# Kernel optimization log

Measured on AMD Instinct MI355X. Metric: run time of the kernel, lower is better.

## Reference

```python
import jax, jax.numpy as jnp
import numpy as np

N, E, SEQ, IN, HID, OUT = 2048, 65536, 5, 32, 64, 16
EPS = 1e-5


def setup_inputs() -> dict:
    ks = jax.random.split(jax.random.key(0), 16)
    def w(k, shape):
        return jax.random.normal(k, shape, jnp.float32) / np.float32(np.sqrt(shape[0]))
    z = lambda n: jnp.zeros((n,), jnp.float32)
    return dict(
        x=jax.random.normal(ks[0], (SEQ, N, IN), jnp.float32),
        edge_weight=jax.random.uniform(ks[1], (E,), jnp.float32),
        Wcz=w(ks[2], (IN, HID)), bcz=z(HID), Wlz=w(ks[3], (2 * HID, HID)), blz=z(HID),
        Wcr=w(ks[4], (IN, HID)), bcr=z(HID), Wlr=w(ks[5], (2 * HID, HID)), blr=z(HID),
        Wch=w(ks[6], (IN, HID)), bch=z(HID), Wlh=w(ks[7], (2 * HID, HID)), blh=z(HID),
        Wred=w(ks[8], (SEQ * HID, HID)), bred=z(HID),
        Wc1=w(ks[9], (HID, HID)), bc1=z(HID), Wc2=w(ks[10], (HID, HID)), bc2=z(HID),
        g1=jnp.ones((HID,), jnp.float32), be1=z(HID),
        g2=jnp.ones((HID,), jnp.float32), be2=z(HID),
        Wout=w(ks[11], (HID, OUT)), bout=z(OUT),
        Wi1=w(ks[12], (2 * HID, HID)), bi1=z(HID),
        Wi2=w(ks[13], (HID, 1)), bi2=z(1),
        edge_index=jax.random.randint(ks[14], (2, E), 0, N),
    )


def _layer_norm(h, g, b):
    mu = jnp.mean(h, -1, keepdims=True)
    var = jnp.mean((h - mu) ** 2, -1, keepdims=True)
    return (h - mu) * jax.lax.rsqrt(var + EPS) * g + b


def _forward(x, edge_weight, Wcz, bcz, Wlz, blz, Wcr, bcr, Wlr, blr,
             Wch, bch, Wlh, blh, Wred, bred, Wc1, bc1, Wc2, bc2,
             g1, be1, g2, be2, Wout, bout, Wi1, bi1, Wi2, bi2, edge_index):
    src, dst = edge_index[0], edge_index[1]
    # GCN symmetric normalization with self-loops (weight 1.0); shared by all convs.
    deg = jax.ops.segment_sum(edge_weight, dst, num_segments=N) + 1.0
    dinv = jax.lax.rsqrt(deg)
    norm = dinv[src] * edge_weight * dinv[dst]  # [E]
    dself = dinv * dinv                          # [N] self-loop coefficient

    def gcn(h, W, b):
        hw = h @ W
        agg = jax.ops.segment_sum(norm[:, None] * hw[src], dst, num_segments=N)
        return agg + dself[:, None] * hw + b

    # TGCN per timestep. The original passes no hidden state, so H resets to 0
    # each call: H_t = (1 - Z) * tanh(candidate); reset gate R is multiplied by
    # H=0 and has no effect (its params get zero gradient, matching torch).
    hs = []
    for t in range(SEQ):  # SEQ=5, fixed small loop
        Zg = jax.nn.sigmoid(gcn(x[t], Wcz, bcz) @ Wlz[:HID] + blz)
        Ht = jnp.tanh(gcn(x[t], Wch, bch) @ Wlh[:HID] + blh)
        hs.append((1.0 - Zg) * Ht)
    h = jnp.stack(hs, axis=1).reshape(N, SEQ * HID)
    h = h @ Wred + bred
    emb = h  # intermediate embeddings for the interaction predictor
    h = gcn(h, Wc1, bc1)
    h = jax.nn.relu(_layer_norm(h, g1, be1))  # dropout = identity in eval
    h = gcn(h, Wc2, bc2)
    h = jax.nn.relu(_layer_norm(h, g2, be2))
    node_pred = h @ Wout + bout
    # InteractionPredictor: cat([e_i, e_j]) @ Wi1 == e_i @ Wi1[:H] + e_j @ Wi1[H:]
    a = emb @ Wi1[:HID]
    bj = emb @ Wi1[HID:]
    hp = jax.nn.relu(a[:, None, :] + bj[None, :, :] + bi1)  # [N, N, HID]
    scores = (hp @ Wi2)[..., 0] + bi2[0]                     # [N, N]
    return node_pred, scores


def reference(x, edge_index, edge_weight, Wcz, bcz, Wlz, blz, Wcr, bcr, Wlr, blr,
              Wch, bch, Wlh, blh, Wred, bred, Wc1, bc1, Wc2, bc2,
              g1, be1, g2, be2, Wout, bout, Wi1, bi1, Wi2, bi2):
    return _forward(x, edge_weight, Wcz, bcz, Wlz, blz, Wcr, bcr, Wlr, blr,
                    Wch, bch, Wlh, blh, Wred, bred, Wc1, bc1, Wc2, bc2,
                    g1, be1, g2, be2, Wout, bout, Wi1, bi1, Wi2, bi2, edge_index)
```

## Files before the change

### kernel.cpp

```cpp
#include <hip/hip_runtime.h>
#include <math.h>

#define N_NODES 2048
#define N_EDGES 65536
#define SEQL 5
#define IN_F 32
#define HID 64
#define OUT_F 16
#define LN_EPS 1e-5f

__global__ __launch_bounds__(256) void k_deg_wcomb(
        const int* __restrict__ ei, const float* __restrict__ ew,
        const float* __restrict__ Wcz, const float* __restrict__ Wlz,
        const float* __restrict__ bcz, const float* __restrict__ blz,
        const float* __restrict__ Wch, const float* __restrict__ Wlh,
        const float* __restrict__ bch, const float* __restrict__ blh,
        float* __restrict__ deg, int* __restrict__ cnt,
        float* __restrict__ Wzp, float* __restrict__ Whp, float* __restrict__ bUV){
    int b = blockIdx.x, t = threadIdx.x;
    if (b < 256){
        int e = b * 256 + t;
        int d = ei[N_EDGES + e];
        atomicAdd(&deg[d], ew[e]);
        atomicAdd(&cnt[d], 1);
    } else {
        const float* Wc = (b == 256) ? Wcz : Wch;
        const float* Wl = (b == 256) ? Wlz : Wlh;
        const float* bc = (b == 256) ? bcz : bch;
        const float* bl = (b == 256) ? blz : blh;
        float* Wp = (b == 256) ? Wzp : Whp;
        for (int idx = t; idx < IN_F*HID; idx += 256){
            int i = idx >> 6, f = idx & 63;
            float s = 0.f;
            #pragma unroll 8
            for (int k = 0; k < HID; ++k) s += Wc[i*HID+k] * Wl[k*HID+f];
            Wp[idx] = s;
        }
        if (t < HID){
            float s = bl[t];
            for (int k = 0; k < HID; ++k) s += bc[k] * Wl[k*HID+t];
            bUV[(b-256)*HID + t] = s;
        }
    }
}

__global__ __launch_bounds__(1024) void k_scan(
        const float* __restrict__ deg, const int* __restrict__ cnt,
        int* __restrict__ rowptr, float* __restrict__ dinv, float* __restrict__ dself,
        int* __restrict__ fill){
    __shared__ int sc[1024];
    int t = threadIdx.x;
    int c0 = cnt[2*t], c1 = cnt[2*t+1];
    int ts = c0 + c1;
    sc[t] = ts;
    __syncthreads();
    for (int off = 1; off < 1024; off <<= 1){
        int v = (t >= off) ? sc[t - off] : 0;
        __syncthreads();
        sc[t] += v;
        __syncthreads();
    }
    int exc = sc[t] - ts;
    rowptr[2*t]   = exc;
    rowptr[2*t+1] = exc + c0;
    if (t == 1023) rowptr[N_NODES] = sc[t];
    float i0 = 1.f / sqrtf(deg[2*t] + 1.f);
    float i1 = 1.f / sqrtf(deg[2*t+1] + 1.f);
    dinv[2*t] = i0;     dinv[2*t+1] = i1;
    dself[2*t] = i0*i0; dself[2*t+1] = i1*i1;
    fill[2*t] = 0;      fill[2*t+1] = 0;
}

__global__ void k_csr(const int* __restrict__ ei, const float* __restrict__ ew,
                      const float* __restrict__ dinv, const int* __restrict__ rowptr,
                      int* __restrict__ fill, int* __restrict__ csrc, float* __restrict__ cnrm){
    int e = blockIdx.x * 256 + threadIdx.x;
    if (e < N_EDGES){
        int s = ei[e], d = ei[N_EDGES + e];
        int pos = rowptr[d] + atomicAdd(&fill[d], 1);
        csrc[pos] = s;
        cnrm[pos] = dinv[s] * ew[e] * dinv[d];
    }
}

__global__ __launch_bounds__(320) void k_gate(const float* __restrict__ x,
        const float* __restrict__ dself, const int* __restrict__ rowptr,
        const int* __restrict__ csrc, const float* __restrict__ cnrm,
        const float* __restrict__ bUV, const float* __restrict__ Wzp, const float* __restrict__ Whp,
        const float* __restrict__ Wred, const float* __restrict__ bred,
        const float* __restrict__ Wi1, const float* __restrict__ bi1, const float* __restrict__ Wc1,
        float* __restrict__ ag, float* __restrict__ bjp, float* __restrict__ hw1){
    int n = blockIdx.x;
    int tid = threadIdx.x;
    __shared__ float part[10][SEQL][IN_F];
    __shared__ float axs[SEQL][IN_F];
    __shared__ float hs[SEQL][HID];
    __shared__ float pw[SEQL][HID];
    __shared__ float hemb[HID];
    const int slot = tid >> 5, f5 = tid & 31;
    const int f = tid & 63, t = tid >> 6;
    int beg = rowptr[n], end = rowptr[n+1];
    float a0=0.f, a1=0.f, a2=0.f, a3=0.f, a4=0.f;
    for (int p = beg + slot; p < end; p += 10){
        int s = csrc[p]; float c = cnrm[p];
        a0 += c * x[(0*N_NODES + s)*IN_F + f5];
        a1 += c * x[(1*N_NODES + s)*IN_F + f5];
        a2 += c * x[(2*N_NODES + s)*IN_F + f5];
        a3 += c * x[(3*N_NODES + s)*IN_F + f5];
        a4 += c * x[(4*N_NODES + s)*IN_F + f5];
    }
    part[slot][0][f5] = a0;
    part[slot][1][f5] = a1;
    part[slot][2][f5] = a2;
    part[slot][3][f5] = a3;
    part[slot][4][f5] = a4;
    __syncthreads();
    if (tid < SEQL*IN_F){
        int tt = tid >> 5, ff = tid & 31;
        float s = dself[n] * x[(tt*N_NODES + n)*IN_F + ff];
        #pragma unroll
        for (int sl = 0; sl < 10; ++sl) s += part[sl][tt][ff];
        axs[tt][ff] = s;
    }
    __syncthreads();
    {
        float zz = bUV[f], hh = bUV[HID + f];
        #pragma unroll
        for (int i = 0; i < IN_F; ++i){
            float a = axs[t][i];
            zz += a * Wzp[i*HID + f];
            hh += a * Whp[i*HID + f];
        }
        float z = 1.f / (1.f + expf(-zz));
        hs[t][f] = (1.f - z) * tanhf(hh);
    }
    __syncthreads();
    {   float pp = 0.f;
        #pragma unroll
        for (int k = 0; k < HID; ++k) pp += hs[t][k] * Wred[(t*HID + k)*HID + f];
        pw[t][f] = pp;
    }
    __syncthreads();
    if (tid < HID){
        float hr = bred[tid];
        #pragma unroll
        for (int t2 = 0; t2 < SEQL; ++t2) hr += pw[t2][tid];
        hemb[tid] = hr;
    }
    __syncthreads();
    if (t < 3){
        const float* W = (t == 0) ? Wi1 : (t == 1) ? (Wi1 + HID*HID) : Wc1;
        float acc = (t == 1) ? bi1[f] : 0.f;
        #pragma unroll
        for (int k = 0; k < HID; ++k) acc += hemb[k] * W[k*HID + f];
        float* O = (t == 0) ? ag : (t == 1) ? bjp : hw1;
        O[n*HID + f] = acc;
    }
}

__global__ __launch_bounds__(256) void k_gcn1(
                       const float* __restrict__ hw1, const float* __restrict__ dself,
                       const int* __restrict__ rowptr, const int* __restrict__ csrc, const float* __restrict__ cnrm,
                       const float* __restrict__ bc1, const float* __restrict__ g1, const float* __restrict__ be1,
                       const float* __restrict__ Wc2, float* __restrict__ hw2){
    int n = blockIdx.x;
    int f = threadIdx.x & 63;
    int w = threadIdx.x >> 6;
    int beg = rowptr[n], end = rowptr[n+1];
    __shared__ float red[4][HID];
    __shared__ float hsh[HID];
    float agg = 0.f;
    for (int p = beg + w; p < end; p += 4) agg += cnrm[p] * hw1[csrc[p]*HID + f];
    red[w][f] = agg;
    __syncthreads();
    if (w == 0){
        float g = red[0][f] + red[1][f] + red[2][f] + red[3][f]
                + dself[n] * hw1[n*HID + f] + bc1[f];
        float sum = g;
        for (int o = 32; o > 0; o >>= 1) sum += __shfl_xor(sum, o, 64);
        float mu = sum * (1.f/64.f);
        float d = g - mu;
        float vs = d * d;
        for (int o = 32; o > 0; o >>= 1) vs += __shfl_xor(vs, o, 64);
        float var = vs * (1.f/64.f);
        float h = d * (1.f / sqrtf(var + LN_EPS)) * g1[f] + be1[f];
        hsh[f] = fmaxf(h, 0.f);
    }
    __syncthreads();
    float s = 0.f;
    #pragma unroll
    for (int k = 0; k < 16; ++k) s += hsh[w*16 + k] * Wc2[(w*16 + k)*HID + f];
    red[w][f] = s;
    __syncthreads();
    if (w == 0) hw2[n*HID + f] = red[0][f] + red[1][f] + red[2][f] + red[3][f];
}

__global__ __launch_bounds__(256) void k_gcn2s(
        const float* __restrict__ hw2, const float* __restrict__ dself,
        const int* __restrict__ rowptr, const int* __restrict__ csrc, const float* __restrict__ cnrm,
        const float* __restrict__ bc2, const float* __restrict__ g2, const float* __restrict__ be2,
        const float* __restrict__ Wout, const float* __restrict__ bout,
        const float* __restrict__ ag, const float* __restrict__ bjp,
        const float* __restrict__ Wi2, const float* __restrict__ bi2,
        float* __restrict__ outp, float* __restrict__ outs){
    int blk = blockIdx.x;
    int tid = threadIdx.x;
    if (blk < N_NODES){
        __shared__ float red[4][HID];
        __shared__ float hsh[HID];
        int n = blk;
        int f = tid & 63;
        int w = tid >> 6;
        int beg = rowptr[n], end = rowptr[n+1];
        float agg = 0.f;
        for (int p = beg + w; p < end; p += 4) agg += cnrm[p] * hw2[csrc[p]*HID + f];
        red[w][f] = agg;
        __syncthreads();
        if (w == 0){
            float g = red[0][f] + red[1][f] + red[2][f] + red[3][f]
                    + dself[n] * hw2[n*HID + f] + bc2[f];
            float sum = g;
            for (int o = 32; o > 0; o >>= 1) sum += __shfl_xor(sum, o, 64);
            float mu = sum * (1.f/64.f);
            float d = g - mu;
            float vs = d * d;
            for (int o = 32; o > 0; o >>= 1) vs += __shfl_xor(vs, o, 64);
            float var = vs * (1.f/64.f);
            float h = d * (1.f / sqrtf(var + LN_EPS)) * g2[f] + be2[f];
            hsh[f] = fmaxf(h, 0.f);
        }
        __syncthreads();
        if (w == 0 && f < OUT_F){
            float s = bout[f];
            #pragma unroll
            for (int k = 0; k < HID; ++k) s += hsh[k] * Wout[k*OUT_F + f];
            outp[n*OUT_F + f] = s;
        }
    } else {
        __shared__ float bs[64*65];
        __shared__ float wv[64];
        int tl = blk - N_NODES;
        int j0 = (tl & 31) * 64;
        int i0 = (tl >> 5) * 16;
        for (int idx = tid; idx < 4096; idx += 256){
            int jj = idx >> 6, f = idx & 63;
            bs[jj*65 + f] = bjp[(j0 + jj)*HID + f];
        }
        if (tid < 64) wv[tid] = Wi2[tid];
        __syncthreads();
        int tj = tid & 63;
        int w = __builtin_amdgcn_readfirstlane(tid >> 6);
        const float* ar = ag + (i0 + w*4)*HID;
        float bi2v = bi2[0];
        float acc0 = 0.f, acc1 = 0.f, acc2 = 0.f, acc3 = 0.f;
        #pragma unroll
        for (int f = 0; f < 64; ++f){
            float bv = bs[tj*65 + f];
            float wf = wv[f];
            acc0 += fmaxf(ar[       f] + bv, 0.f) * wf;
            acc1 += fmaxf(ar[ 64 +  f] + bv, 0.f) * wf;
            acc2 += fmaxf(ar[128 +  f] + bv, 0.f) * wf;
            acc3 += fmaxf(ar[192 +  f] + bv, 0.f) * wf;
        }
        long ro = (long)(i0 + w*4) * N_NODES + j0 + tj;
        outs[ro                ] = acc0 + bi2v;
        outs[ro +     N_NODES  ] = acc1 + bi2v;
        outs[ro + 2L* N_NODES  ] = acc2 + bi2v;
        outs[ro + 3L* N_NODES  ] = acc3 + bi2v;
    }
}

extern "C" void kernel_launch(void* const* d_in, const int* in_sizes, int n_in,
                              void* d_out, int out_size, void* d_ws, size_t ws_size,
                              hipStream_t stream){
    const float* x   = (const float*)d_in[0];
    const float* ew  = (const float*)d_in[1];
    const float* Wcz = (const float*)d_in[2];  const float* bcz = (const float*)d_in[3];
    const float* Wlz = (const float*)d_in[4];  const float* blz = (const float*)d_in[5];
    const float* Wch = (const float*)d_in[10]; const float* bch = (const float*)d_in[11];
    const float* Wlh = (const float*)d_in[12]; const float* blh = (const float*)d_in[13];
    const float* Wred= (const float*)d_in[14]; const float* bred= (const float*)d_in[15];
    const float* Wc1 = (const float*)d_in[16]; const float* bc1 = (const float*)d_in[17];
    const float* Wc2 = (const float*)d_in[18]; const float* bc2 = (const float*)d_in[19];
    const float* g1  = (const float*)d_in[20]; const float* be1 = (const float*)d_in[21];
    const float* g2  = (const float*)d_in[22]; const float* be2 = (const float*)d_in[23];
    const float* Wout= (const float*)d_in[24]; const float* bout= (const float*)d_in[25];
    const float* Wi1 = (const float*)d_in[26]; const float* bi1 = (const float*)d_in[27];
    const float* Wi2 = (const float*)d_in[28]; const float* bi2 = (const float*)d_in[29];
    const int*  ei  = (const int*)d_in[30];

    float* w = (float*)d_ws;
    float* deg    = w;
    int*   cnt    = (int*)(w + 2048);
    int*   rowptr = (int*)(w + 4096);
    float* dinv   = w + 6656;
    float* dself  = w + 8704;
    int*   fill   = (int*)(w + 10752);
    int*   csrc   = (int*)(w + 12800);
    float* cnrm   = w + 78336;
    float* Wzp    = w + 143872;
    float* Whp    = w + 145920;
    float* bUV    = w + 147968;
    float* ag     = w + 148096;
    float* bjp    = w + 279168;
    float* hw1    = w + 410240;
    float* hw2    = w + 541312;

    hipMemsetAsync(deg, 0, 16384, stream);
    k_deg_wcomb<<<258, 256, 0, stream>>>(ei, ew, Wcz, Wlz, bcz, blz, Wch, Wlh, bch, blh,
                                         deg, cnt, Wzp, Whp, bUV);
    k_scan<<<1, 1024, 0, stream>>>(deg, cnt, rowptr, dinv, dself, fill);
    k_csr<<<N_EDGES/256, 256, 0, stream>>>(ei, ew, dinv, rowptr, fill, csrc, cnrm);
    k_gate<<<N_NODES, 320, 0, stream>>>(x, dself, rowptr, csrc, cnrm, bUV, Wzp, Whp,
                                        Wred, bred, Wi1, bi1, Wc1, ag, bjp, hw1);
    k_gcn1<<<N_NODES, 256, 0, stream>>>(hw1, dself, rowptr, csrc, cnrm, bc1, g1, be1, Wc2, hw2);
    k_gcn2s<<<N_NODES + 4096, 256, 0, stream>>>(hw2, dself, rowptr, csrc, cnrm,
                                                bc2, g2, be2, Wout, bout,
                                                ag, bjp, Wi2, bi2,
                                                (float*)d_out, (float*)d_out + N_NODES*OUT_F);
}
```

Baseline: 221.7 us.

## Pack CSR edges as float2 and vectorize neighbor gathers with float4 across more slots

Interleaves each CSR entry's source index and normalization into a single float2, so one load fetches both. The gate and both GCN aggregation loops now gather neighbor features as float4 and spread each node's edges over many more slots (40 or 32 instead of 10 or 4). This raises memory-level parallelism for the roughly 32-neighbor rows, at the cost of a longer shared-memory reduction. The GCN and score kernels move to 512-thread blocks, with the score tiles doubled in rows so half as many blocks are launched.

```diff
diff --git a/kernel.cpp b/kernel.cpp
--- a/kernel.cpp
+++ b/kernel.cpp
@@ -73,53 +73,62 @@
 
 __global__ void k_csr(const int* __restrict__ ei, const float* __restrict__ ew,
                       const float* __restrict__ dinv, const int* __restrict__ rowptr,
-                      int* __restrict__ fill, int* __restrict__ csrc, float* __restrict__ cnrm){
+                      int* __restrict__ fill, float2* __restrict__ cedge){
     int e = blockIdx.x * 256 + threadIdx.x;
     if (e < N_EDGES){
         int s = ei[e], d = ei[N_EDGES + e];
         int pos = rowptr[d] + atomicAdd(&fill[d], 1);
-        csrc[pos] = s;
-        cnrm[pos] = dinv[s] * ew[e] * dinv[d];
+        float2 v;
+        v.x = __int_as_float(s);
+        v.y = dinv[s] * ew[e] * dinv[d];
+        cedge[pos] = v;
     }
 }
 
 __global__ __launch_bounds__(320) void k_gate(const float* __restrict__ x,
         const float* __restrict__ dself, const int* __restrict__ rowptr,
-        const int* __restrict__ csrc, const float* __restrict__ cnrm,
+        const float2* __restrict__ cedge,
         const float* __restrict__ bUV, const float* __restrict__ Wzp, const float* __restrict__ Whp,
         const float* __restrict__ Wred, const float* __restrict__ bred,
         const float* __restrict__ Wi1, const float* __restrict__ bi1, const float* __restrict__ Wc1,
         float* __restrict__ ag, float* __restrict__ bjp, float* __restrict__ hw1){
     int n = blockIdx.x;
     int tid = threadIdx.x;
-    __shared__ float part[10][SEQL][IN_F];
+    __shared__ float part[40*SEQL*IN_F];
     __shared__ float axs[SEQL][IN_F];
     __shared__ float hs[SEQL][HID];
     __shared__ float pw[SEQL][HID];
     __shared__ float hemb[HID];
-    const int slot = tid >> 5, f5 = tid & 31;
+    const int slot = tid >> 3, fl = tid & 7;
     const int f = tid & 63, t = tid >> 6;
     int beg = rowptr[n], end = rowptr[n+1];
-    float a0=0.f, a1=0.f, a2=0.f, a3=0.f, a4=0.f;
-    for (int p = beg + slot; p < end; p += 10){
-        int s = csrc[p]; float c = cnrm[p];
-        a0 += c * x[(0*N_NODES + s)*IN_F + f5];
-        a1 += c * x[(1*N_NODES + s)*IN_F + f5];
-        a2 += c * x[(2*N_NODES + s)*IN_F + f5];
-        a3 += c * x[(3*N_NODES + s)*IN_F + f5];
-        a4 += c * x[(4*N_NODES + s)*IN_F + f5];
-    }
-    part[slot][0][f5] = a0;
-    part[slot][1][f5] = a1;
-    part[slot][2][f5] = a2;
-    part[slot][3][f5] = a3;
-    part[slot][4][f5] = a4;
+    const float4* X4 = (const float4*)x;
+    float4 a0 = {0,0,0,0}, a1 = {0,0,0,0}, a2 = {0,0,0,0}, a3 = {0,0,0,0}, a4 = {0,0,0,0};
+    for (int p = beg + slot; p < end; p += 40){
+        float2 ed = cedge[p];
+        int s = __float_as_int(ed.x); float c = ed.y;
+        float4 x0 = X4[(0*N_NODES + s)*8 + fl];
+        float4 x1 = X4[(1*N_NODES + s)*8 + fl];
+        float4 x2 = X4[(2*N_NODES + s)*8 + fl];
+        float4 x3 = X4[(3*N_NODES + s)*8 + fl];
+        float4 x4v= X4[(4*N_NODES + s)*8 + fl];
+        a0.x += c*x0.x; a0.y += c*x0.y; a0.z += c*x0.z; a0.w += c*x0.w;
+        a1.x += c*x1.x; a1.y += c*x1.y; a1.z += c*x1.z; a1.w += c*x1.w;
+        a2.x += c*x2.x; a2.y += c*x2.y; a2.z += c*x2.z; a2.w += c*x2.w;
+        a3.x += c*x3.x; a3.y += c*x3.y; a3.z += c*x3.z; a3.w += c*x3.w;
+        a4.x += c*x4v.x; a4.y += c*x4v.y; a4.z += c*x4v.z; a4.w += c*x4v.w;
+    }
+    *(float4*)&part[(slot*SEQL + 0)*IN_F + fl*4] = a0;
+    *(float4*)&part[(slot*SEQL + 1)*IN_F + fl*4] = a1;
+    *(float4*)&part[(slot*SEQL + 2)*IN_F + fl*4] = a2;
+    *(float4*)&part[(slot*SEQL + 3)*IN_F + fl*4] = a3;
+    *(float4*)&part[(slot*SEQL + 4)*IN_F + fl*4] = a4;
     __syncthreads();
     if (tid < SEQL*IN_F){
         int tt = tid >> 5, ff = tid & 31;
         float s = dself[n] * x[(tt*N_NODES + n)*IN_F + ff];
-        #pragma unroll
-        for (int sl = 0; sl < 10; ++sl) s += part[sl][tt][ff];
+        #pragma unroll 8
+        for (int sl = 0; sl < 40; ++sl) s += part[(sl*SEQL + tt)*IN_F + ff];
         axs[tt][ff] = s;
     }
     __syncthreads();
@@ -158,24 +167,33 @@
     }
 }
 
-__global__ __launch_bounds__(256) void k_gcn1(
-                       const float* __restrict__ hw1, const float* __restrict__ dself,
-                       const int* __restrict__ rowptr, const int* __restrict__ csrc, const float* __restrict__ cnrm,
-                       const float* __restrict__ bc1, const float* __restrict__ g1, const float* __restrict__ be1,
-                       const float* __restrict__ Wc2, float* __restrict__ hw2){
+__global__ __launch_bounds__(512) void k_gcn1(
+        const float* __restrict__ hw1, const float* __restrict__ dself,
+        const int* __restrict__ rowptr, const float2* __restrict__ cedge,
+        const float* __restrict__ bc1, const float* __restrict__ g1, const float* __restrict__ be1,
+        const float* __restrict__ Wc2, float* __restrict__ hw2){
     int n = blockIdx.x;
-    int f = threadIdx.x & 63;
-    int w = threadIdx.x >> 6;
+    int tid = threadIdx.x;
+    __shared__ float part[32*HID];
+    __shared__ float hsh[HID];
+    __shared__ float red8[8*HID];
+    const int slot = tid >> 4, fl = tid & 15;
+    const int f = tid & 63, w = tid >> 6;
     int beg = rowptr[n], end = rowptr[n+1];
-    __shared__ float red[4][HID];
-    __shared__ float hsh[HID];
-    float agg = 0.f;
-    for (int p = beg + w; p < end; p += 4) agg += cnrm[p] * hw1[csrc[p]*HID + f];
-    red[w][f] = agg;
+    const float4* H4 = (const float4*)hw1;
+    float4 acc = {0,0,0,0};
+    for (int p = beg + slot; p < end; p += 32){
+        float2 ed = cedge[p];
+        int s = __float_as_int(ed.x); float c = ed.y;
+        float4 h = H4[s*16 + fl];
+        acc.x += c*h.x; acc.y += c*h.y; acc.z += c*h.z; acc.w += c*h.w;
+    }
+    *(float4*)&part[slot*HID + fl*4] = acc;
     __syncthreads();
     if (w == 0){
-        float g = red[0][f] + red[1][f] + red[2][f] + red[3][f]
-                + dself[n] * hw1[n*HID + f] + bc1[f];
+        float g = bc1[f] + dself[n] * hw1[n*HID + f];
+        #pragma unroll 8
+        for (int sl = 0; sl < 32; ++sl) g += part[sl*HID + f];
         float sum = g;
         for (int o = 32; o > 0; o >>= 1) sum += __shfl_xor(sum, o, 64);
         float mu = sum * (1.f/64.f);
@@ -189,15 +207,20 @@
     __syncthreads();
     float s = 0.f;
     #pragma unroll
-    for (int k = 0; k < 16; ++k) s += hsh[w*16 + k] * Wc2[(w*16 + k)*HID + f];
-    red[w][f] = s;
-    __syncthreads();
-    if (w == 0) hw2[n*HID + f] = red[0][f] + red[1][f] + red[2][f] + red[3][f];
-}
-
-__global__ __launch_bounds__(256) void k_gcn2s(
+    for (int k = 0; k < 8; ++k) s += hsh[w*8 + k] * Wc2[(w*8 + k)*HID + f];
+    red8[w*HID + f] = s;
+    __syncthreads();
+    if (w == 0){
+        float o = 0.f;
+        #pragma unroll
+        for (int k = 0; k < 8; ++k) o += red8[k*HID + f];
+        hw2[n*HID + f] = o;
+    }
+}
+
+__global__ __launch_bounds__(512) void k_gcn2s(
         const float* __restrict__ hw2, const float* __restrict__ dself,
-        const int* __restrict__ rowptr, const int* __restrict__ csrc, const float* __restrict__ cnrm,
+        const int* __restrict__ rowptr, const float2* __restrict__ cedge,
         const float* __restrict__ bc2, const float* __restrict__ g2, const float* __restrict__ be2,
         const float* __restrict__ Wout, const float* __restrict__ bout,
         const float* __restrict__ ag, const float* __restrict__ bjp,
@@ -206,19 +229,26 @@
     int blk = blockIdx.x;
     int tid = threadIdx.x;
     if (blk < N_NODES){
-        __shared__ float red[4][HID];
+        __shared__ float part[32*HID];
         __shared__ float hsh[HID];
         int n = blk;
-        int f = tid & 63;
-        int w = tid >> 6;
+        const int slot = tid >> 4, fl = tid & 15;
+        const int f = tid & 63, w = tid >> 6;
         int beg = rowptr[n], end = rowptr[n+1];
-        float agg = 0.f;
-        for (int p = beg + w; p < end; p += 4) agg += cnrm[p] * hw2[csrc[p]*HID + f];
-        red[w][f] = agg;
+        const float4* H4 = (const float4*)hw2;
+        float4 acc = {0,0,0,0};
+        for (int p = beg + slot; p < end; p += 32){
+            float2 ed = cedge[p];
+            int s = __float_as_int(ed.x); float c = ed.y;
+            float4 h = H4[s*16 + fl];
+            acc.x += c*h.x; acc.y += c*h.y; acc.z += c*h.z; acc.w += c*h.w;
+        }
+        *(float4*)&part[slot*HID + fl*4] = acc;
         __syncthreads();
         if (w == 0){
-            float g = red[0][f] + red[1][f] + red[2][f] + red[3][f]
-                    + dself[n] * hw2[n*HID + f] + bc2[f];
+            float g = bc2[f] + dself[n] * hw2[n*HID + f];
+            #pragma unroll 8
+            for (int sl = 0; sl < 32; ++sl) g += part[sl*HID + f];
             float sum = g;
             for (int o = 32; o > 0; o >>= 1) sum += __shfl_xor(sum, o, 64);
             float mu = sum * (1.f/64.f);
@@ -241,8 +271,8 @@
         __shared__ float wv[64];
         int tl = blk - N_NODES;
         int j0 = (tl & 31) * 64;
-        int i0 = (tl >> 5) * 16;
-        for (int idx = tid; idx < 4096; idx += 256){
+        int i0 = (tl >> 5) * 32;
+        for (int idx = tid; idx < 4096; idx += 512){
             int jj = idx >> 6, f = idx & 63;
             bs[jj*65 + f] = bjp[(j0 + jj)*HID + f];
         }
@@ -296,8 +326,7 @@
     float* dinv   = w + 6656;
     float* dself  = w + 8704;
     int*   fill   = (int*)(w + 10752);
-    int*   csrc   = (int*)(w + 12800);
-    float* cnrm   = w + 78336;
+    float2* cedge = (float2*)(w + 12800);
     float* Wzp    = w + 143872;
     float* Whp    = w + 145920;
     float* bUV    = w + 147968;
@@ -310,11 +339,11 @@
     k_deg_wcomb<<<258, 256, 0, stream>>>(ei, ew, Wcz, Wlz, bcz, blz, Wch, Wlh, bch, blh,
                                          deg, cnt, Wzp, Whp, bUV);
     k_scan<<<1, 1024, 0, stream>>>(deg, cnt, rowptr, dinv, dself, fill);
-    k_csr<<<N_EDGES/256, 256, 0, stream>>>(ei, ew, dinv, rowptr, fill, csrc, cnrm);
-    k_gate<<<N_NODES, 320, 0, stream>>>(x, dself, rowptr, csrc, cnrm, bUV, Wzp, Whp,
+    k_csr<<<N_EDGES/256, 256, 0, stream>>>(ei, ew, dinv, rowptr, fill, cedge);
+    k_gate<<<N_NODES, 320, 0, stream>>>(x, dself, rowptr, cedge, bUV, Wzp, Whp,
                                         Wred, bred, Wi1, bi1, Wc1, ag, bjp, hw1);
-    k_gcn1<<<N_NODES, 256, 0, stream>>>(hw1, dself, rowptr, csrc, cnrm, bc1, g1, be1, Wc2, hw2);
-    k_gcn2s<<<N_NODES + 4096, 256, 0, stream>>>(hw2, dself, rowptr, csrc, cnrm,
+    k_gcn1<<<N_NODES, 512, 0, stream>>>(hw1, dself, rowptr, cedge, bc1, g1, be1, Wc2, hw2);
+    k_gcn2s<<<N_NODES + 2048, 512, 0, stream>>>(hw2, dself, rowptr, cedge,
                                                 bc2, g2, be2, Wout, bout,
                                                 ag, bjp, Wi2, bi2,
                                                 (float*)d_out, (float*)d_out + N_NODES*OUT_F);
```

Result: faster. 217.0 us (-2.1%).
